# Kernel optimization log

Measured on AMD Instinct MI355X. Metric: run time of the kernel, lower is better.

## Reference

```python
import jax, jax.numpy as jnp
import numpy as np

B, L, ENC_IN, DM, H, HD, DFF, NL, C_OUT = 4, 1024, 64, 512, 8, 64, 2048, 3, 64
SCALE = 1.0 / np.sqrt(HD)


def _ln(x, g, b):
    m = x.mean(-1, keepdims=True)
    v = ((x - m) ** 2).mean(-1, keepdims=True)
    return (x - m) / jnp.sqrt(v + 1e-5) * g + b


def _pos_encoding(length, d):
    pos = np.arange(length)[:, None].astype(np.float32)
    div = np.exp(np.arange(0, d, 2).astype(np.float32) * (-np.log(10000.0) / d))
    pe = np.zeros((length, d), np.float32)
    pe[:, 0::2] = np.sin(pos * div)
    pe[:, 1::2] = np.cos(pos * div)
    return jnp.asarray(pe)

PE = _pos_encoding(L, DM)


def _prob_attn(q, k, v, idx):
    # q,k,v: [B,H,L,D]; idx: [L, sample_k] random key indices per query
    qk = jnp.einsum('bhqd,bhkd->bhqk', q, k)                       # [B,H,L,L]
    qks = jnp.take_along_axis(qk, idx[None, None, :, :], axis=-1)   # sampled QK
    M = qks.max(-1) - qks.sum(-1) / L                                # sparsity measure [B,H,L]
    _, top = jax.lax.top_k(M, L)  # n_top == L here (degenerate full selection / permutation)
    scores = jnp.take_along_axis(qk, top[..., None], axis=2) * SCALE  # gathered Q rows
    A = jax.nn.softmax(scores, axis=-1)
    return jnp.einsum('bhuk,bhkd->bhud', A, v)                       # [B,H,L,D]


def _forward(x_enc, sample_idx, W_emb, b_emb, Wq, bq, Wk, bk, Wv, bv, Wo, bo,
             W1, b1, W2, b2, g1, be1, g2, be2, gN, bN, W_proj, b_proj):
    x = x_enc @ W_emb + b_emb + PE[None]  # [B,L,DM]
    for i in range(NL):
        q = (x @ Wq[i] + bq[i]).reshape(B, L, H, HD).transpose(0, 2, 1, 3)
        k = (x @ Wk[i] + bk[i]).reshape(B, L, H, HD).transpose(0, 2, 1, 3)
        v = (x @ Wv[i] + bv[i]).reshape(B, L, H, HD).transpose(0, 2, 1, 3)
        o = _prob_attn(q, k, v, sample_idx[i]).transpose(0, 2, 1, 3).reshape(B, L, DM)
        o = o @ Wo[i] + bo[i]
        x = _ln(x + o, g1[i], be1[i])
        y = jax.nn.gelu(x @ W1[i] + b1[i], approximate=False) @ W2[i] + b2[i]
        x = _ln(x + y, g2[i], be2[i])
    x = _ln(x, gN, bN)
    return x @ W_proj + b_proj


def setup_inputs() -> dict:
    key = jax.random.key(0)
    ks = jax.random.split(key, 16)
    nrm = lambda k, s: jax.random.normal(k, s, jnp.float32) * 0.02
    return {
        'x_enc': jax.random.normal(ks[0], (B, L, ENC_IN), jnp.float32),
        'sample_idx': jax.random.randint(ks[1], (NL, L, L), 0, L, dtype=jnp.int32),
        'W_emb': nrm(ks[2], (ENC_IN, DM)), 'b_emb': jnp.zeros((DM,), jnp.float32),
        'Wq': nrm(ks[3], (NL, DM, DM)), 'bq': jnp.zeros((NL, DM), jnp.float32),
        'Wk': nrm(ks[4], (NL, DM, DM)), 'bk': jnp.zeros((NL, DM), jnp.float32),
        'Wv': nrm(ks[5], (NL, DM, DM)), 'bv': jnp.zeros((NL, DM), jnp.float32),
        'Wo': nrm(ks[6], (NL, DM, DM)), 'bo': jnp.zeros((NL, DM), jnp.float32),
        'W1': nrm(ks[7], (NL, DM, DFF)), 'b1': jnp.zeros((NL, DFF), jnp.float32),
        'W2': nrm(ks[8], (NL, DFF, DM)), 'b2': jnp.zeros((NL, DM), jnp.float32),
        'g1': jnp.ones((NL, DM), jnp.float32), 'be1': jnp.zeros((NL, DM), jnp.float32),
        'g2': jnp.ones((NL, DM), jnp.float32), 'be2': jnp.zeros((NL, DM), jnp.float32),
        'gN': jnp.ones((DM,), jnp.float32), 'bN': jnp.zeros((DM,), jnp.float32),
        'W_proj': nrm(ks[9], (DM, C_OUT)), 'b_proj': jnp.zeros((C_OUT,), jnp.float32),
    }


def reference(x_enc, sample_idx, W_emb, b_emb, Wq, bq, Wk, bk, Wv, bv, Wo, bo,
              W1, b1, W2, b2, g1, be1, g2, be2, gN, bN, W_proj, b_proj):
    return _forward(x_enc, sample_idx, W_emb, b_emb, Wq, bq, Wk, bk, Wv, bv, Wo, bo,
                    W1, b1, W2, b2, g1, be1, g2, be2, gN, bN, W_proj, b_proj)
```

## Files before the change

### kernel.cpp

```cpp
#include <hip/hip_runtime.h>
#include <cstdint>
#include <cstddef>

#define B_    4
#define L_    1024
#define ENCIN 64
#define DM    512
#define H_    8
#define HD    64
#define DFF   2048
#define NL    3
#define COUT  64
#define SCALE 0.125f
#define BH    32

typedef __attribute__((ext_vector_type(4))) short short4v;
typedef __attribute__((ext_vector_type(8))) short short8v;
typedef __attribute__((ext_vector_type(4))) float f32x4;
typedef unsigned short u16;

#define MFMA16(a,b,c) __builtin_amdgcn_mfma_f32_16x16x32_bf16(a,b,c,0,0,0)

#define GL2LDS(gsrc, ldst) \
  __builtin_amdgcn_global_load_lds( \
      (const __attribute__((address_space(1))) void*)(uintptr_t)(const void*)(gsrc), \
      (__attribute__((address_space(3))) void*)(uintptr_t)(const void*)(ldst), 16, 0, 0)

__device__ __forceinline__ u16 f2bf(float f){
  unsigned u = __float_as_uint(f);
  u += 0x7fffu + ((u >> 16) & 1u);
  return (u16)(u >> 16);
}
__device__ __forceinline__ float bf2f(u16 h){
  return __uint_as_float(((unsigned)h) << 16);
}
__device__ __forceinline__ void split2(float v, u16* h, u16* l){
  u16 hh = f2bf(v);
  *h = hh;
  *l = f2bf(v - bf2f(hh));
}

template<int MODE>
__global__ __launch_bounds__(256) void hgemm(
    const u16* __restrict__ Ah, const u16* __restrict__ Al,
    const u16* __restrict__ Bh, const u16* __restrict__ Bl,
    const float* __restrict__ bias1, const float* __restrict__ bias2,
    const float* __restrict__ bias3,
    float* __restrict__ o32, u16* __restrict__ oh, u16* __restrict__ ol,
    u16* __restrict__ oh2, u16* __restrict__ ol2, u16* __restrict__ ov,
    int Mtot, int N, int K, int klen)
{
  __shared__ u16 As[2][2][128*32];
  __shared__ u16 Bs[2][2][64*32];
  const int t = threadIdx.x, lane = t & 63, wid = t >> 6;
  const int wr = wid >> 1, wc = wid & 1;
  const int fr = lane & 15, fq = lane >> 4;
  const int m0 = blockIdx.y * 128, n0 = blockIdx.x * 64;
  const int z = blockIdx.z;
  const int kbase = z * klen;
  const int srow = lane >> 2, sseg = lane & 3;

  const int nk = klen / 32;

  auto stage = [&](int buf, int kt) {
#pragma unroll
    for (int i = 0; i < 2; i++) {
      int c = wid + 4*i;
      GL2LDS(&Ah[(size_t)(m0 + c*16 + srow)*K + kt + sseg*8], &As[buf][0][c*512]);
      GL2LDS(&Al[(size_t)(m0 + c*16 + srow)*K + kt + sseg*8], &As[buf][1][c*512]);
    }
    {
      int c = wid;
      GL2LDS(&Bh[(size_t)(n0 + c*16 + srow)*K + kt + sseg*8], &Bs[buf][0][c*512]);
      GL2LDS(&Bl[(size_t)(n0 + c*16 + srow)*K + kt + sseg*8], &Bs[buf][1][c*512]);
    }
  };

  f32x4 acc[4][2] = {};
  stage(0, kbase);
  __syncthreads();

  for (int it = 0; it < nk; ++it) {
    int cur = it & 1;
    if (it + 1 < nk) stage(cur ^ 1, kbase + (it+1)*32);

    short8v a0[4], a1[4], b0[2], b1[2];
#pragma unroll
    for (int m = 0; m < 4; m++) {
      int off = (wr*64 + m*16 + fr)*32 + fq*4;
      short4v x0 = *(const short4v*)&As[cur][0][off];
      short4v x1 = *(const short4v*)&As[cur][0][off + 16];
      a0[m] = __builtin_shufflevector(x0, x1, 0,1,2,3,4,5,6,7);
      short4v y0 = *(const short4v*)&As[cur][1][off];
      short4v y1 = *(const short4v*)&As[cur][1][off + 16];
      a1[m] = __builtin_shufflevector(y0, y1, 0,1,2,3,4,5,6,7);
    }
#pragma unroll
    for (int n = 0; n < 2; n++) {
      int off = (wc*32 + n*16 + fr)*32 + fq*4;
      short4v x0 = *(const short4v*)&Bs[cur][0][off];
      short4v x1 = *(const short4v*)&Bs[cur][0][off + 16];
      b0[n] = __builtin_shufflevector(x0, x1, 0,1,2,3,4,5,6,7);
      short4v y0 = *(const short4v*)&Bs[cur][1][off];
      short4v y1 = *(const short4v*)&Bs[cur][1][off + 16];
      b1[n] = __builtin_shufflevector(y0, y1, 0,1,2,3,4,5,6,7);
    }
#pragma unroll
    for (int m = 0; m < 4; m++)
#pragma unroll
      for (int n = 0; n < 2; n++) {
        acc[m][n] = MFMA16(a0[m], b0[n], acc[m][n]);
        acc[m][n] = MFMA16(a0[m], b1[n], acc[m][n]);
        acc[m][n] = MFMA16(a1[m], b0[n], acc[m][n]);
      }
    __syncthreads();
  }

#pragma unroll
  for (int m = 0; m < 4; m++) {
#pragma unroll
    for (int n = 0; n < 2; n++) {
      int gc = n0 + wc*32 + n*16 + fr;
#pragma unroll
      for (int r = 0; r < 4; r++) {
        int row = m0 + wr*64 + m*16 + fq*4 + r;
        float v = acc[m][n][r];
        if (MODE == 5) {
          o32[((size_t)z*Mtot + row)*N + gc] = v;
        } else if (MODE == 0) {
          o32[(size_t)row*N + gc] = v + bias1[gc];
        } else if (MODE == 1) {
          v += bias1[gc];
          int li = row & (L_ - 1);
          float dv = expf((float)(gc & ~1) * -0.017988946039015984f);
          float ang = (float)li * dv;
          v += (gc & 1) ? cosf(ang) : sinf(ang);
          size_t ix = (size_t)row*N + gc;
          o32[ix] = v;
          split2(v, &oh[ix], &ol[ix]);
        } else if (MODE == 2) {
          v += bias1[gc];
          float gv = 0.5f * v * (1.0f + erff(v * 0.70710678118654752f));
          size_t ix = (size_t)row*N + gc;
          split2(gv, &oh[ix], &ol[ix]);
        } else if (MODE == 3) {
          int b = row >> 10, li = row & (L_ - 1);
          int sub = gc >> 9, h = (gc >> 6) & 7, d = gc & 63;
          if (sub == 0) {
            v += bias1[gc];
            size_t ix = (((size_t)(b*H_ + h))*L_ + li)*HD + d;
            split2(v, &oh[ix], &ol[ix]);
          } else if (sub == 1) {
            v += bias2[gc - 512];
            size_t ix = (((size_t)(b*H_ + h))*L_ + li)*HD + d;
            split2(v, &oh2[ix], &ol2[ix]);
          } else {
            v += bias3[gc - 1024];
            size_t ix = (((size_t)(b*H_ + h))*HD + d)*L_ + li;
            ov[ix] = f2bf(v);
          }
        }
      }
    }
  }
}

__global__ __launch_bounds__(256) void qk_mfma(
    const u16* __restrict__ qh, const u16* __restrict__ ql,
    const u16* __restrict__ kh, const u16* __restrict__ kl,
    float* __restrict__ S, float* __restrict__ pmax, float* __restrict__ psum)
{
  __shared__ u16 Qs0[128*64], Qs1[128*64], Ks0[128*64], Ks1[128*64];
  const int t = threadIdx.x, lane = t & 63, wid = t >> 6;
  const int wr = wid >> 1, wc = wid & 1;
  const int fr = lane & 15, fq = lane >> 4;
  const int n0 = blockIdx.x * 128, m0 = blockIdx.y * 128, bh = blockIdx.z;
  const int srow = lane >> 3, sseg = lane & 7;
  const u16* qhb = qh + (size_t)bh * L_ * HD;
  const u16* qlb = ql + (size_t)bh * L_ * HD;
  const u16* khb = kh + (size_t)bh * L_ * HD;
  const u16* klb = kl + (size_t)bh * L_ * HD;

#pragma unroll
  for (int i = 0; i < 4; i++) {
    int c = wid + 4*i;
    GL2LDS(&qhb[(size_t)(m0 + c*8 + srow)*HD + sseg*8], &Qs0[c*512]);
    GL2LDS(&qlb[(size_t)(m0 + c*8 + srow)*HD + sseg*8], &Qs1[c*512]);
    GL2LDS(&khb[(size_t)(n0 + c*8 + srow)*HD + sseg*8], &Ks0[c*512]);
    GL2LDS(&klb[(size_t)(n0 + c*8 + srow)*HD + sseg*8], &Ks1[c*512]);
  }
  __syncthreads();

  f32x4 acc[4][4] = {};
#pragma unroll
  for (int ks = 0; ks < 2; ks++) {
    int kg = ks*32 + fq*4;
    short8v a0[4], a1[4], b0[4], b1[4];
#pragma unroll
    for (int m = 0; m < 4; m++) {
      int off = (wr*64 + m*16 + fr)*64 + kg;
      short4v x0 = *(const short4v*)&Qs0[off];
      short4v x1 = *(const short4v*)&Qs0[off + 16];
      a0[m] = __builtin_shufflevector(x0, x1, 0,1,2,3,4,5,6,7);
      short4v y0 = *(const short4v*)&Qs1[off];
      short4v y1 = *(const short4v*)&Qs1[off + 16];
      a1[m] = __builtin_shufflevector(y0, y1, 0,1,2,3,4,5,6,7);
    }
#pragma unroll
    for (int n = 0; n < 4; n++) {
      int off = (wc*64 + n*16 + fr)*64 + kg;
      short4v x0 = *(const short4v*)&Ks0[off];
      short4v x1 = *(const short4v*)&Ks0[off + 16];
      b0[n] = __builtin_shufflevector(x0, x1, 0,1,2,3,4,5,6,7);
      short4v y0 = *(const short4v*)&Ks1[off];
      short4v y1 = *(const short4v*)&Ks1[off + 16];
      b1[n] = __builtin_shufflevector(y0, y1, 0,1,2,3,4,5,6,7);
    }
#pragma unroll
    for (int m = 0; m < 4; m++)
#pragma unroll
      for (int n = 0; n < 4; n++) {
        acc[m][n] = MFMA16(a0[m], b0[n], acc[m][n]);
        acc[m][n] = MFMA16(a0[m], b1[n], acc[m][n]);
        acc[m][n] = MFMA16(a1[m], b0[n], acc[m][n]);
      }
  }

#pragma unroll
  for (int m = 0; m < 4; m++)
#pragma unroll
    for (int n = 0; n < 4; n++)
#pragma unroll
      for (int r = 0; r < 4; r++) {
        int grow = m0 + wr*64 + m*16 + fq*4 + r;
        int gcol = n0 + wc*64 + n*16 + fr;
        S[((size_t)bh*L_ + grow)*L_ + gcol] = acc[m][n][r];
      }

  const int tix = blockIdx.x*2 + wc;
#pragma unroll
  for (int m = 0; m < 4; m++) {
    float mx[4], sm[4];
#pragma unroll
    for (int r = 0; r < 4; r++) {
      float v = fmaxf(fmaxf(acc[m][0][r], acc[m][1][r]),
                      fmaxf(acc[m][2][r], acc[m][3][r]));
#pragma unroll
      for (int o2 = 1; o2 < 16; o2 <<= 1) v = fmaxf(v, __shfl_xor(v, o2));
      mx[r] = v * SCALE;
      float s = 0.f;
#pragma unroll
      for (int n = 0; n < 4; n++) s += expf(acc[m][n][r]*SCALE - mx[r]);
#pragma unroll
      for (int o2 = 1; o2 < 16; o2 <<= 1) s += __shfl_xor(s, o2);
      sm[r] = s;
    }
    if (fr == 0) {
#pragma unroll
      for (int r = 0; r < 4; r++) {
        int grow = m0 + wr*64 + m*16 + fq*4 + r;
        size_t ix = ((size_t)bh*L_ + grow)*16 + tix;
        pmax[ix] = mx[r];
        psum[ix] = sm[r];
      }
    }
  }
}

__global__ __launch_bounds__(256) void smc_k(const float* __restrict__ pmax,
    const float* __restrict__ psum, float* __restrict__ rmx, float* __restrict__ rsm)
{
  const int g = threadIdx.x & 15;
  const size_t flat = (size_t)blockIdx.x*16 + (threadIdx.x >> 4);
  float m = pmax[flat*16 + g], s = psum[flat*16 + g];
  float gm = m;
#pragma unroll
  for (int o = 1; o < 16; o <<= 1) gm = fmaxf(gm, __shfl_xor(gm, o));
  float gs = s * expf(m - gm);
#pragma unroll
  for (int o = 1; o < 16; o <<= 1) gs += __shfl_xor(gs, o);
  if (g == 0) { rmx[flat] = gm; rsm[flat] = gs; }
}

__global__ __launch_bounds__(256) void m_k(const float* __restrict__ S,
    const int* __restrict__ idx, float* __restrict__ Mv)
{
  const int qi = blockIdx.x, bh = blockIdx.y, t = threadIdx.x;
  const float* row = S + ((size_t)bh * L_ + qi) * L_;
  const int* ir = idx + (size_t)qi * L_;
  float mx = -1e30f, sm = 0.f;
  for (int s = t; s < L_; s += 256) {
    float v = row[ir[s]];
    mx = fmaxf(mx, v);
    sm += v;
  }
#pragma unroll
  for (int o = 32; o > 0; o >>= 1) {
    mx = fmaxf(mx, __shfl_xor(mx, o));
    sm += __shfl_xor(sm, o);
  }
  __shared__ float wmx[4], wsm[4];
  if ((t & 63) == 0) { wmx[t >> 6] = mx; wsm[t >> 6] = sm; }
  __syncthreads();
  if (t == 0) {
    mx = fmaxf(fmaxf(wmx[0], wmx[1]), fmaxf(wmx[2], wmx[3]));
    sm = wsm[0] + wsm[1] + wsm[2] + wsm[3];
    Mv[(size_t)bh * L_ + qi] = mx - sm * (1.0f / L_);
  }
}

__global__ __launch_bounds__(1024) void sort_k(const float* __restrict__ Mv,
                                               int* __restrict__ rank)
{
  __shared__ unsigned long long keys[L_];
  const int bh = blockIdx.x, t = threadIdx.x;
  float m = Mv[(size_t)bh * L_ + t];
  unsigned u = __float_as_uint(m);
  u = (u & 0x80000000u) ? ~u : (u | 0x80000000u);
  keys[t] = ((unsigned long long)(~u) << 32) | (unsigned)t;
  __syncthreads();
  for (int k = 2; k <= L_; k <<= 1) {
    for (int j = k >> 1; j > 0; j >>= 1) {
      int ixj = t ^ j;
      if (ixj > t) {
        unsigned long long a = keys[t], b = keys[ixj];
        bool up = ((t & k) == 0);
        if ((a > b) == up) { keys[t] = b; keys[ixj] = a; }
      }
      __syncthreads();
    }
  }
  int orig = (int)(keys[t] & 0xFFFFFFFFu);
  rank[(size_t)bh * L_ + orig] = t;
}

__global__ __launch_bounds__(256) void pv_mfma(
    const float* __restrict__ S, const u16* __restrict__ vt,
    const float* __restrict__ rmx, const float* __restrict__ rsm,
    const int* __restrict__ rank,
    u16* __restrict__ ath, u16* __restrict__ atl)
{
  __shared__ u16 Ps[64*64];
  __shared__ u16 Vs[64*64];
  __shared__ float rmaxS[64], rsumS[64];
  __shared__ int rankS[64];
  const int t = threadIdx.x, lane = t & 63, wid = t >> 6;
  const int wr = wid >> 1, wc = wid & 1;
  const int fr = lane & 15, fq = lane >> 4;
  const int l0 = blockIdx.x * 64, bh = blockIdx.y;
  const int bb = bh >> 3, hh = bh & 7;
  const int srow = lane >> 3, sseg = lane & 7;

  if (t < 64) {
    rmaxS[t] = rmx[(size_t)bh*L_ + l0 + t];
    rsumS[t] = rsm[(size_t)bh*L_ + l0 + t];
    rankS[t] = rank[(size_t)bh*L_ + l0 + t];
  }
  __syncthreads();

  f32x4 acc[2][2] = {};
  for (int c0 = 0; c0 < L_; c0 += 64) {
#pragma unroll
    for (int i = 0; i < 2; i++) {
      int c = wid + 4*i;
      GL2LDS(&vt[((size_t)bh*HD + c*8 + srow)*L_ + c0 + sseg*8], &Vs[c*512]);
    }
#pragma unroll
    for (int i = 0; i < 4; i++) {
      int f = t + 256*i;
      int row = f >> 4, q = f & 15;
      float4 s4 = *(const float4*)&S[((size_t)bh*L_ + l0 + row)*L_ + c0 + q*4];
      float mxr = rmaxS[row];
      short4v p4 = { (short)f2bf(expf(s4.x*SCALE - mxr)),
                     (short)f2bf(expf(s4.y*SCALE - mxr)),
                     (short)f2bf(expf(s4.z*SCALE - mxr)),
                     (short)f2bf(expf(s4.w*SCALE - mxr)) };
      *(short4v*)&Ps[row*64 + q*4] = p4;
    }
    __syncthreads();
#pragma unroll
    for (int ks = 0; ks < 2; ks++) {
      int kg = ks*32 + fq*4;
      short8v a[2], b[2];
#pragma unroll
      for (int m = 0; m < 2; m++) {
        int off = (wr*32 + m*16 + fr)*64 + kg;
        short4v x0 = *(const short4v*)&Ps[off];
        short4v x1 = *(const short4v*)&Ps[off + 16];
        a[m] = __builtin_shufflevector(x0, x1, 0,1,2,3,4,5,6,7);
      }
#pragma unroll
      for (int n = 0; n < 2; n++) {
        int off = (wc*32 + n*16 + fr)*64 + kg;
        short4v x0 = *(const short4v*)&Vs[off];
        short4v x1 = *(const short4v*)&Vs[off + 16];
        b[n] = __builtin_shufflevector(x0, x1, 0,1,2,3,4,5,6,7);
      }
#pragma unroll
      for (int m = 0; m < 2; m++)
#pragma unroll
        for (int n = 0; n < 2; n++)
          acc[m][n] = MFMA16(a[m], b[n], acc[m][n]);
    }
    __syncthreads();
  }

#pragma unroll
  for (int m = 0; m < 2; m++)
#pragma unroll
    for (int n = 0; n < 2; n++)
#pragma unroll
      for (int r = 0; r < 4; r++) {
        int lrow = wr*32 + m*16 + fq*4 + r;
        int u = rankS[lrow];
        int d = wc*32 + n*16 + fr;
        float o = acc[m][n][r] / rsumS[lrow];
        size_t ix = ((size_t)bb*L_ + u)*DM + hh*HD + d;
        split2(o, &ath[ix], &atl[ix]);
      }
}

__global__ __launch_bounds__(64) void ln2_k(const float* __restrict__ xin,
    const float* __restrict__ part, int np, const float* __restrict__ bias,
    const float* __restrict__ g, const float* __restrict__ bb,
    float* __restrict__ out, u16* __restrict__ oh, u16* __restrict__ ol)
{
  const int row = blockIdx.x, t = threadIdx.x;
  const float4* xf = (const float4*)(xin + (size_t)row * DM);
  float4 v0 = xf[t], v1 = xf[t + 64];
  for (int p = 0; p < np; p++) {
    const float4* af = (const float4*)(part + ((size_t)p*(B_*L_) + row) * DM);
    float4 a0 = af[t], a1 = af[t + 64];
    v0.x += a0.x; v0.y += a0.y; v0.z += a0.z; v0.w += a0.w;
    v1.x += a1.x; v1.y += a1.y; v1.z += a1.z; v1.w += a1.w;
  }
  if (bias) {
    const float4* cf = (const float4*)bias;
    float4 c0 = cf[t], c1 = cf[t + 64];
    v0.x += c0.x; v0.y += c0.y; v0.z += c0.z; v0.w += c0.w;
    v1.x += c1.x; v1.y += c1.y; v1.z += c1.z; v1.w += c1.w;
  }
  float s  = v0.x + v0.y + v0.z + v0.w + v1.x + v1.y + v1.z + v1.w;
  float ss = v0.x*v0.x + v0.y*v0.y + v0.z*v0.z + v0.w*v0.w +
             v1.x*v1.x + v1.y*v1.y + v1.z*v1.z + v1.w*v1.w;
#pragma unroll
  for (int o = 32; o > 0; o >>= 1) { s += __shfl_xor(s, o); ss += __shfl_xor(ss, o); }
  float mean = s * (1.0f / DM);
  float var  = ss * (1.0f / DM) - mean * mean;
  float inv  = 1.0f / sqrtf(var + 1e-5f);
  const float4* gf = (const float4*)g;
  const float4* bf = (const float4*)bb;
  float4 g0 = gf[t], g1 = gf[t + 64], b0 = bf[t], b1 = bf[t + 64];
  float o0[4], o1[4];
  o0[0] = (v0.x-mean)*inv*g0.x + b0.x; o0[1] = (v0.y-mean)*inv*g0.y + b0.y;
  o0[2] = (v0.z-mean)*inv*g0.z + b0.z; o0[3] = (v0.w-mean)*inv*g0.w + b0.w;
  o1[0] = (v1.x-mean)*inv*g1.x + b1.x; o1[1] = (v1.y-mean)*inv*g1.y + b1.y;
  o1[2] = (v1.z-mean)*inv*g1.z + b1.z; o1[3] = (v1.w-mean)*inv*g1.w + b1.w;
  float4* of = (float4*)(out + (size_t)row * DM);
  of[t]      = make_float4(o0[0], o0[1], o0[2], o0[3]);
  of[t + 64] = make_float4(o1[0], o1[1], o1[2], o1[3]);
  size_t base = (size_t)row * DM;
#pragma unroll
  for (int j = 0; j < 4; j++) {
    split2(o0[j], &oh[base + t*4 + j],       &ol[base + t*4 + j]);
    split2(o1[j], &oh[base + 256 + t*4 + j], &ol[base + 256 + t*4 + j]);
  }
}

__global__ __launch_bounds__(256) void wt_k(const float* __restrict__ W,
    u16* __restrict__ Th, u16* __restrict__ Tl, int K, int N,
    size_t wz, size_t tz)
{
  W  += (size_t)blockIdx.z * wz;
  Th += (size_t)blockIdx.z * tz;
  Tl += (size_t)blockIdx.z * tz;
  __shared__ float tile[32][33];
  const int k0 = blockIdx.y * 32, n0 = blockIdx.x * 32;
  const int c = threadIdx.x & 31, r4 = threadIdx.x >> 5;
#pragma unroll
  for (int i = 0; i < 4; i++) {
    int r = r4 * 4 + i;
    tile[r][c] = W[(size_t)(k0 + r) * N + n0 + c];
  }
  __syncthreads();
#pragma unroll
  for (int i = 0; i < 4; i++) {
    int r = r4 * 4 + i;
    float v = tile[c][r];
    split2(v, &Th[(size_t)(n0 + r) * K + k0 + c], &Tl[(size_t)(n0 + r) * K + k0 + c]);
  }
}

__global__ __launch_bounds__(256) void split_k(const float* __restrict__ in,
    u16* __restrict__ oh, u16* __restrict__ ol, int n4)
{
  int i = blockIdx.x * 256 + threadIdx.x;
  if (i < n4) {
    float4 v = ((const float4*)in)[i];
    split2(v.x, &oh[i*4+0], &ol[i*4+0]);
    split2(v.y, &oh[i*4+1], &ol[i*4+1]);
    split2(v.z, &oh[i*4+2], &ol[i*4+2]);
    split2(v.w, &oh[i*4+3], &ol[i*4+3]);
  }
}

extern "C" void kernel_launch(void* const* d_in, const int* in_sizes, int n_in,
                              void* d_out, int out_size, void* d_ws, size_t ws_size,
                              hipStream_t stream)
{
  const float* x_enc   = (const float*)d_in[0];
  const int*   sidx    = (const int*)d_in[1];
  const float* W_emb   = (const float*)d_in[2];
  const float* b_emb   = (const float*)d_in[3];
  const float* Wq      = (const float*)d_in[4];
  const float* bq      = (const float*)d_in[5];
  const float* Wk      = (const float*)d_in[6];
  const float* bk      = (const float*)d_in[7];
  const float* Wv      = (const float*)d_in[8];
  const float* bv      = (const float*)d_in[9];
  const float* Wo      = (const float*)d_in[10];
  const float* bo      = (const float*)d_in[11];
  const float* W1      = (const float*)d_in[12];
  const float* b1      = (const float*)d_in[13];
  const float* W2      = (const float*)d_in[14];
  const float* b2      = (const float*)d_in[15];
  const float* g1      = (const float*)d_in[16];
  const float* be1     = (const float*)d_in[17];
  const float* g2      = (const float*)d_in[18];
  const float* be2     = (const float*)d_in[19];
  const float* gN      = (const float*)d_in[20];
  const float* bN      = (const float*)d_in[21];
  const float* W_proj  = (const float*)d_in[22];
  const float* b_proj  = (const float*)d_in[23];

  const int M = B_ * L_;
  char* w = (char*)d_ws;
  float* S   = (float*)w;  w += (size_t)BH * L_ * L_ * 4;
  float* x   = (float*)w;  w += (size_t)M * DM * 4;
  u16* xh    = (u16*)w;    w += (size_t)M * DM * 2;
  u16* xl    = (u16*)w;    w += (size_t)M * DM * 2;
  u16* qh_   = (u16*)w;    w += (size_t)BH * L_ * HD * 2;
  u16* ql_   = (u16*)w;    w += (size_t)BH * L_ * HD * 2;
  u16* kh_   = (u16*)w;    w += (size_t)BH * L_ * HD * 2;
  u16* kl_   = (u16*)w;    w += (size_t)BH * L_ * HD * 2;
  u16* vt_   = (u16*)w;    w += (size_t)BH * L_ * HD * 2;
  u16* ath   = (u16*)w;    w += (size_t)M * DM * 2;
  u16* atl   = (u16*)w;    w += (size_t)M * DM * 2;
  float* rmx_ = (float*)w; w += (size_t)BH * L_ * 4;
  float* rsm_ = (float*)w; w += (size_t)BH * L_ * 4;
  float* Mv_  = (float*)w; w += (size_t)BH * L_ * 4;
  int* rank_  = (int*)w;   w += (size_t)BH * L_ * 4;
  float* pmax_ = (float*)w; w += (size_t)BH * L_ * 16 * 4;
  float* psum_ = (float*)w; w += (size_t)BH * L_ * 16 * 4;
  u16* WqkvTh = (u16*)w; w += (size_t)NL*1536*DM*2;
  u16* WqkvTl = (u16*)w; w += (size_t)NL*1536*DM*2;
  u16* WoTh   = (u16*)w; w += (size_t)NL*DM*DM*2;
  u16* WoTl   = (u16*)w; w += (size_t)NL*DM*DM*2;
  u16* W1Th   = (u16*)w; w += (size_t)NL*DFF*DM*2;
  u16* W1Tl   = (u16*)w; w += (size_t)NL*DFF*DM*2;
  u16* W2Th   = (u16*)w; w += (size_t)NL*DM*DFF*2;
  u16* W2Tl   = (u16*)w; w += (size_t)NL*DM*DFF*2;
  u16* WeTh   = (u16*)w; w += (size_t)DM*ENCIN*2;
  u16* WeTl   = (u16*)w; w += (size_t)DM*ENCIN*2;
  u16* WpTh   = (u16*)w; w += (size_t)COUT*DM*2;
  u16* WpTl   = (u16*)w; w += (size_t)COUT*DM*2;
  u16*   yh     = (u16*)S;
  u16*   yl     = (u16*)((char*)S + 16u*1024u*1024u);
  float* partWo = (float*)((char*)S + 32u*1024u*1024u);
  float* partW2 = (float*)((char*)S + 48u*1024u*1024u);
  u16*   xeh    = (u16*)((char*)S + 80u*1024u*1024u);
  u16*   xel    = xeh + (size_t)M*ENCIN;

  split_k<<<dim3((M*ENCIN/4 + 255)/256), 256, 0, stream>>>(x_enc, xeh, xel, M*ENCIN/4);
  wt_k<<<dim3(DM/32, DM/32, NL), 256, 0, stream>>>(Wq, WqkvTh,            WqkvTl,            DM, DM, (size_t)DM*DM, (size_t)1536*DM);
  wt_k<<<dim3(DM/32, DM/32, NL), 256, 0, stream>>>(Wk, WqkvTh + 512*DM,   WqkvTl + 512*DM,   DM, DM, (size_t)DM*DM, (size_t)1536*DM);
  wt_k<<<dim3(DM/32, DM/32, NL), 256, 0, stream>>>(Wv, WqkvTh + 1024*DM,  WqkvTl + 1024*DM,  DM, DM, (size_t)DM*DM, (size_t)1536*DM);
  wt_k<<<dim3(DM/32, DM/32, NL), 256, 0, stream>>>(Wo, WoTh, WoTl, DM, DM, (size_t)DM*DM, (size_t)DM*DM);
  wt_k<<<dim3(DFF/32, DM/32, NL), 256, 0, stream>>>(W1, W1Th, W1Tl, DM, DFF, (size_t)DM*DFF, (size_t)DFF*DM);
  wt_k<<<dim3(DM/32, DFF/32, NL), 256, 0, stream>>>(W2, W2Th, W2Tl, DFF, DM, (size_t)DFF*DM, (size_t)DM*DFF);
  wt_k<<<dim3(DM/32, ENCIN/32, 1), 256, 0, stream>>>(W_emb, WeTh, WeTl, ENCIN, DM, 0, 0);
  wt_k<<<dim3(COUT/32, DM/32, 1), 256, 0, stream>>>(W_proj, WpTh, WpTl, DM, COUT, 0, 0);

  hgemm<1><<<dim3(DM/64, M/128, 1), 256, 0, stream>>>(
      xeh, xel, WeTh, WeTl, b_emb, nullptr, nullptr,
      x, xh, xl, nullptr, nullptr, nullptr, M, DM, ENCIN, ENCIN);

  for (int il = 0; il < NL; il++) {
    hgemm<3><<<dim3(1536/64, M/128, 1), 256, 0, stream>>>(
        xh, xl, WqkvTh + (size_t)il*1536*DM, WqkvTl + (size_t)il*1536*DM,
        bq + il*DM, bk + il*DM, bv + il*DM,
        nullptr, qh_, ql_, kh_, kl_, vt_, M, 1536, DM, DM);

    qk_mfma<<<dim3(L_/128, L_/128, BH), 256, 0, stream>>>(qh_, ql_, kh_, kl_, S, pmax_, psum_);
    smc_k<<<dim3(BH*L_/16), 256, 0, stream>>>(pmax_, psum_, rmx_, rsm_);
    m_k<<<dim3(L_, BH), 256, 0, stream>>>(S, sidx + (size_t)il*L_*L_, Mv_);
    sort_k<<<BH, 1024, 0, stream>>>(Mv_, rank_);
    pv_mfma<<<dim3(L_/64, BH), 256, 0, stream>>>(S, vt_, rmx_, rsm_, rank_, ath, atl);

    hgemm<5><<<dim3(DM/64, M/128, 2), 256, 0, stream>>>(
        ath, atl, WoTh + (size_t)il*DM*DM, WoTl + (size_t)il*DM*DM,
        nullptr, nullptr, nullptr,
        partWo, nullptr, nullptr, nullptr, nullptr, nullptr, M, DM, DM, DM/2);
    ln2_k<<<M, 64, 0, stream>>>(x, partWo, 2, bo + il*DM, g1 + il*DM, be1 + il*DM, x, xh, xl);

    hgemm<2><<<dim3(DFF/64, M/128, 1), 256, 0, stream>>>(
        xh, xl, W1Th + (size_t)il*DFF*DM, W1Tl + (size_t)il*DFF*DM,
        b1 + il*DFF, nullptr, nullptr,
        nullptr, yh, yl, nullptr, nullptr, nullptr, M, DFF, DM, DM);
    hgemm<5><<<dim3(DM/64, M/128, 4), 256, 0, stream>>>(
        yh, yl, W2Th + (size_t)il*DM*DFF, W2Tl + (size_t)il*DM*DFF,
        nullptr, nullptr, nullptr,
        partW2, nullptr, nullptr, nullptr, nullptr, nullptr, M, DM, DFF, DFF/4);
    ln2_k<<<M, 64, 0, stream>>>(x, partW2, 4, b2 + il*DM, g2 + il*DM, be2 + il*DM, x, xh, xl);
  }

  ln2_k<<<M, 64, 0, stream>>>(x, nullptr, 0, nullptr, gN, bN, x, xh, xl);
  hgemm<0><<<dim3(COUT/64, M/128, 1), 256, 0, stream>>>(
      xh, xl, WpTh, WpTl, b_proj, nullptr, nullptr,
      (float*)d_out, nullptr, nullptr, nullptr, nullptr, nullptr, M, COUT, DM, DM);
}
```

Before: 1.803 ms.

## Fuse attention into flash-style kernels, widen GEMM tiles, split-K final projection

Replaces the materialized fp32 score matrix with two fused kernels. The first recomputes QK^T per 16-query wave to get online softmax stats and the sampled sparsity measure, using a precomputed per-layer sample-count table. The second recomputes QK^T, applies exp and accumulates PV directly in registers. GEMM tile width becomes a template parameter, set to 128 for the QKV, Wo, W1 and W2 GEMMs, and the final projection uses split-K with a reduce kernel. This removes the large S write/read traffic but computes QK^T twice and reads K/V directly from global memory without LDS staging.

```diff
diff --git a/kernel.cpp b/kernel.cpp
--- a/kernel.cpp
+++ b/kernel.cpp
@@ -18,6 +18,7 @@
 typedef __attribute__((ext_vector_type(8))) short short8v;
 typedef __attribute__((ext_vector_type(4))) float f32x4;
 typedef unsigned short u16;
+typedef unsigned char u8;
 
 #define MFMA16(a,b,c) __builtin_amdgcn_mfma_f32_16x16x32_bf16(a,b,c,0,0,0)
 
@@ -39,8 +40,11 @@
   *h = hh;
   *l = f2bf(v - bf2f(hh));
 }
-
-template<int MODE>
+__device__ __forceinline__ short8v cat8(short4v a, short4v b){
+  return __builtin_shufflevector(a, b, 0,1,2,3,4,5,6,7);
+}
+
+template<int BN, int MODE>
 __global__ __launch_bounds__(256) void hgemm(
     const u16* __restrict__ Ah, const u16* __restrict__ Al,
     const u16* __restrict__ Bh, const u16* __restrict__ Bl,
@@ -50,12 +54,13 @@
     u16* __restrict__ oh2, u16* __restrict__ ol2, u16* __restrict__ ov,
     int Mtot, int N, int K, int klen)
 {
+  constexpr int NT = BN / 32;
   __shared__ u16 As[2][2][128*32];
-  __shared__ u16 Bs[2][2][64*32];
+  __shared__ u16 Bs[2][2][BN*32];
   const int t = threadIdx.x, lane = t & 63, wid = t >> 6;
   const int wr = wid >> 1, wc = wid & 1;
   const int fr = lane & 15, fq = lane >> 4;
-  const int m0 = blockIdx.y * 128, n0 = blockIdx.x * 64;
+  const int m0 = blockIdx.y * 128, n0 = blockIdx.x * BN;
   const int z = blockIdx.z;
   const int kbase = z * klen;
   const int srow = lane >> 2, sseg = lane & 3;
@@ -69,14 +74,15 @@
       GL2LDS(&Ah[(size_t)(m0 + c*16 + srow)*K + kt + sseg*8], &As[buf][0][c*512]);
       GL2LDS(&Al[(size_t)(m0 + c*16 + srow)*K + kt + sseg*8], &As[buf][1][c*512]);
     }
-    {
-      int c = wid;
+#pragma unroll
+    for (int i = 0; i < BN/64; i++) {
+      int c = wid + 4*i;
       GL2LDS(&Bh[(size_t)(n0 + c*16 + srow)*K + kt + sseg*8], &Bs[buf][0][c*512]);
       GL2LDS(&Bl[(size_t)(n0 + c*16 + srow)*K + kt + sseg*8], &Bs[buf][1][c*512]);
     }
   };
 
-  f32x4 acc[4][2] = {};
+  f32x4 acc[4][NT] = {};
   stage(0, kbase);
   __syncthreads();
 
@@ -84,31 +90,23 @@
     int cur = it & 1;
     if (it + 1 < nk) stage(cur ^ 1, kbase + (it+1)*32);
 
-    short8v a0[4], a1[4], b0[2], b1[2];
+    short8v a0[4], a1[4], b0[NT], b1[NT];
 #pragma unroll
     for (int m = 0; m < 4; m++) {
       int off = (wr*64 + m*16 + fr)*32 + fq*4;
-      short4v x0 = *(const short4v*)&As[cur][0][off];
-      short4v x1 = *(const short4v*)&As[cur][0][off + 16];
-      a0[m] = __builtin_shufflevector(x0, x1, 0,1,2,3,4,5,6,7);
-      short4v y0 = *(const short4v*)&As[cur][1][off];
-      short4v y1 = *(const short4v*)&As[cur][1][off + 16];
-      a1[m] = __builtin_shufflevector(y0, y1, 0,1,2,3,4,5,6,7);
-    }
-#pragma unroll
-    for (int n = 0; n < 2; n++) {
-      int off = (wc*32 + n*16 + fr)*32 + fq*4;
-      short4v x0 = *(const short4v*)&Bs[cur][0][off];
-      short4v x1 = *(const short4v*)&Bs[cur][0][off + 16];
-      b0[n] = __builtin_shufflevector(x0, x1, 0,1,2,3,4,5,6,7);
-      short4v y0 = *(const short4v*)&Bs[cur][1][off];
-      short4v y1 = *(const short4v*)&Bs[cur][1][off + 16];
-      b1[n] = __builtin_shufflevector(y0, y1, 0,1,2,3,4,5,6,7);
+      a0[m] = cat8(*(const short4v*)&As[cur][0][off], *(const short4v*)&As[cur][0][off+16]);
+      a1[m] = cat8(*(const short4v*)&As[cur][1][off], *(const short4v*)&As[cur][1][off+16]);
+    }
+#pragma unroll
+    for (int n = 0; n < NT; n++) {
+      int off = (wc*(BN/2) + n*16 + fr)*32 + fq*4;
+      b0[n] = cat8(*(const short4v*)&Bs[cur][0][off], *(const short4v*)&Bs[cur][0][off+16]);
+      b1[n] = cat8(*(const short4v*)&Bs[cur][1][off], *(const short4v*)&Bs[cur][1][off+16]);
     }
 #pragma unroll
     for (int m = 0; m < 4; m++)
 #pragma unroll
-      for (int n = 0; n < 2; n++) {
+      for (int n = 0; n < NT; n++) {
         acc[m][n] = MFMA16(a0[m], b0[n], acc[m][n]);
         acc[m][n] = MFMA16(a0[m], b1[n], acc[m][n]);
         acc[m][n] = MFMA16(a1[m], b0[n], acc[m][n]);
@@ -119,8 +117,8 @@
 #pragma unroll
   for (int m = 0; m < 4; m++) {
 #pragma unroll
-    for (int n = 0; n < 2; n++) {
-      int gc = n0 + wc*32 + n*16 + fr;
+    for (int n = 0; n < NT; n++) {
+      int gc = n0 + wc*(BN/2) + n*16 + fr;
 #pragma unroll
       for (int r = 0; r < 4; r++) {
         int row = m0 + wr*64 + m*16 + fq*4 + r;
@@ -165,147 +163,132 @@
   }
 }
 
-__global__ __launch_bounds__(256) void qk_mfma(
+__global__ __launch_bounds__(256) void cnt_k(const int* __restrict__ sidx,
+                                             u8* __restrict__ cnt)
+{
+  __shared__ unsigned c[L_];
+  const int row = blockIdx.x, il = blockIdx.y, t = threadIdx.x;
+#pragma unroll
+  for (int i = 0; i < 4; i++) c[t + 256*i] = 0;
+  __syncthreads();
+  const int* ir = sidx + ((size_t)il*L_ + row)*L_;
+#pragma unroll
+  for (int i = 0; i < 4; i++) atomicAdd(&c[ir[t + 256*i]], 1u);
+  __syncthreads();
+  u8* out = cnt + ((size_t)il*L_ + row)*L_;
+#pragma unroll
+  for (int i = 0; i < 4; i++) out[t + 256*i] = (u8)c[t + 256*i];
+}
+
+__device__ __forceinline__ void st_tile(
+    const u16* __restrict__ khb, const u16* __restrict__ klb,
+    int ct, int fr, int fq, const short8v Qh[2], const short8v Ql[2],
+    f32x4 sacc[4])
+{
+#pragma unroll
+  for (int ks = 0; ks < 2; ks++) {
+#pragma unroll
+    for (int mi = 0; mi < 4; mi++) {
+      const u16* ph = &khb[(size_t)(ct*64 + mi*16 + fr)*HD + ks*32 + fq*4];
+      short8v ah = cat8(*(const short4v*)ph, *(const short4v*)(ph + 16));
+      const u16* pl = &klb[(size_t)(ct*64 + mi*16 + fr)*HD + ks*32 + fq*4];
+      short8v al = cat8(*(const short4v*)pl, *(const short4v*)(pl + 16));
+      sacc[mi] = MFMA16(ah, Qh[ks], sacc[mi]);
+      sacc[mi] = MFMA16(ah, Ql[ks], sacc[mi]);
+      sacc[mi] = MFMA16(al, Qh[ks], sacc[mi]);
+    }
+  }
+}
+
+__device__ __forceinline__ void load_qfrags(
+    const u16* __restrict__ qhb, const u16* __restrict__ qlb,
+    int fr, int fq, short8v Qh[2], short8v Ql[2])
+{
+#pragma unroll
+  for (int ks = 0; ks < 2; ks++) {
+    const u16* p = &qhb[fr*HD + ks*32 + fq*4];
+    Qh[ks] = cat8(*(const short4v*)p, *(const short4v*)(p + 16));
+    const u16* p2 = &qlb[fr*HD + ks*32 + fq*4];
+    Ql[ks] = cat8(*(const short4v*)p2, *(const short4v*)(p2 + 16));
+  }
+}
+
+__device__ __forceinline__ void fdecode(int bid, int w, int& bh, int& q0)
+{
+  int xcd = bid & 7, ii = bid >> 3;
+  bh = xcd*4 + (ii >> 4);
+  q0 = (ii & 15)*64 + w*16;
+}
+
+__global__ __launch_bounds__(256) void fqk_stat(
     const u16* __restrict__ qh, const u16* __restrict__ ql,
     const u16* __restrict__ kh, const u16* __restrict__ kl,
-    float* __restrict__ S, float* __restrict__ pmax, float* __restrict__ psum)
-{
-  __shared__ u16 Qs0[128*64], Qs1[128*64], Ks0[128*64], Ks1[128*64];
-  const int t = threadIdx.x, lane = t & 63, wid = t >> 6;
-  const int wr = wid >> 1, wc = wid & 1;
+    const u8* __restrict__ cnt,
+    float* __restrict__ rmx, float* __restrict__ rsm, float* __restrict__ Mv)
+{
+  const int t = threadIdx.x, lane = t & 63, w = t >> 6;
   const int fr = lane & 15, fq = lane >> 4;
-  const int n0 = blockIdx.x * 128, m0 = blockIdx.y * 128, bh = blockIdx.z;
-  const int srow = lane >> 3, sseg = lane & 7;
-  const u16* qhb = qh + (size_t)bh * L_ * HD;
-  const u16* qlb = ql + (size_t)bh * L_ * HD;
-  const u16* khb = kh + (size_t)bh * L_ * HD;
-  const u16* klb = kl + (size_t)bh * L_ * HD;
-
-#pragma unroll
-  for (int i = 0; i < 4; i++) {
-    int c = wid + 4*i;
-    GL2LDS(&qhb[(size_t)(m0 + c*8 + srow)*HD + sseg*8], &Qs0[c*512]);
-    GL2LDS(&qlb[(size_t)(m0 + c*8 + srow)*HD + sseg*8], &Qs1[c*512]);
-    GL2LDS(&khb[(size_t)(n0 + c*8 + srow)*HD + sseg*8], &Ks0[c*512]);
-    GL2LDS(&klb[(size_t)(n0 + c*8 + srow)*HD + sseg*8], &Ks1[c*512]);
-  }
-  __syncthreads();
-
-  f32x4 acc[4][4] = {};
-#pragma unroll
-  for (int ks = 0; ks < 2; ks++) {
-    int kg = ks*32 + fq*4;
-    short8v a0[4], a1[4], b0[4], b1[4];
-#pragma unroll
-    for (int m = 0; m < 4; m++) {
-      int off = (wr*64 + m*16 + fr)*64 + kg;
-      short4v x0 = *(const short4v*)&Qs0[off];
-      short4v x1 = *(const short4v*)&Qs0[off + 16];
-      a0[m] = __builtin_shufflevector(x0, x1, 0,1,2,3,4,5,6,7);
-      short4v y0 = *(const short4v*)&Qs1[off];
-      short4v y1 = *(const short4v*)&Qs1[off + 16];
-      a1[m] = __builtin_shufflevector(y0, y1, 0,1,2,3,4,5,6,7);
-    }
-#pragma unroll
-    for (int n = 0; n < 4; n++) {
-      int off = (wc*64 + n*16 + fr)*64 + kg;
-      short4v x0 = *(const short4v*)&Ks0[off];
-      short4v x1 = *(const short4v*)&Ks0[off + 16];
-      b0[n] = __builtin_shufflevector(x0, x1, 0,1,2,3,4,5,6,7);
-      short4v y0 = *(const short4v*)&Ks1[off];
-      short4v y1 = *(const short4v*)&Ks1[off + 16];
-      b1[n] = __builtin_shufflevector(y0, y1, 0,1,2,3,4,5,6,7);
-    }
-#pragma unroll
-    for (int m = 0; m < 4; m++)
-#pragma unroll
-      for (int n = 0; n < 4; n++) {
-        acc[m][n] = MFMA16(a0[m], b0[n], acc[m][n]);
-        acc[m][n] = MFMA16(a0[m], b1[n], acc[m][n]);
-        acc[m][n] = MFMA16(a1[m], b0[n], acc[m][n]);
+  int bh, q0; fdecode(blockIdx.x, w, bh, q0);
+  const u16* qhb = qh + ((size_t)bh*L_ + q0)*HD;
+  const u16* qlb = ql + ((size_t)bh*L_ + q0)*HD;
+  const u16* khb = kh + (size_t)bh*L_*HD;
+  const u16* klb = kl + (size_t)bh*L_*HD;
+  const u8* crow = cnt + (size_t)(q0 + fr)*L_;
+
+  short8v Qh[2], Ql[2];
+  load_qfrags(qhb, qlb, fr, fq, Qh, Ql);
+
+  float run_m = -1e30f, run_s = 0.f, smp_m = -1e30f, wsum = 0.f;
+
+#pragma unroll 4
+  for (int ct = 0; ct < 16; ct++) {
+    f32x4 sacc[4] = {};
+    st_tile(khb, klb, ct, fr, fq, Qh, Ql, sacc);
+
+    float tmax = sacc[0][0];
+#pragma unroll
+    for (int mi = 0; mi < 4; mi++)
+#pragma unroll
+      for (int r = 0; r < 4; r++) tmax = fmaxf(tmax, sacc[mi][r]);
+    float zm = tmax * SCALE;
+    float tsum = 0.f;
+#pragma unroll
+    for (int mi = 0; mi < 4; mi++)
+#pragma unroll
+      for (int r = 0; r < 4; r++) tsum += expf(sacc[mi][r]*SCALE - zm);
+    float nm = fmaxf(run_m, zm);
+    run_s = run_s*expf(run_m - nm) + tsum*expf(zm - nm);
+    run_m = nm;
+
+#pragma unroll
+    for (int mi = 0; mi < 4; mi++) {
+      unsigned cw = *(const unsigned*)&crow[ct*64 + mi*16 + fq*4];
+#pragma unroll
+      for (int r = 0; r < 4; r++) {
+        float cf = (float)((cw >> (8*r)) & 255u);
+        float s = sacc[mi][r];
+        wsum += cf * s;
+        if (cf > 0.f) smp_m = fmaxf(smp_m, s);
       }
-  }
-
-#pragma unroll
-  for (int m = 0; m < 4; m++)
-#pragma unroll
-    for (int n = 0; n < 4; n++)
-#pragma unroll
-      for (int r = 0; r < 4; r++) {
-        int grow = m0 + wr*64 + m*16 + fq*4 + r;
-        int gcol = n0 + wc*64 + n*16 + fr;
-        S[((size_t)bh*L_ + grow)*L_ + gcol] = acc[m][n][r];
-      }
-
-  const int tix = blockIdx.x*2 + wc;
-#pragma unroll
-  for (int m = 0; m < 4; m++) {
-    float mx[4], sm[4];
-#pragma unroll
-    for (int r = 0; r < 4; r++) {
-      float v = fmaxf(fmaxf(acc[m][0][r], acc[m][1][r]),
-                      fmaxf(acc[m][2][r], acc[m][3][r]));
-#pragma unroll
-      for (int o2 = 1; o2 < 16; o2 <<= 1) v = fmaxf(v, __shfl_xor(v, o2));
-      mx[r] = v * SCALE;
-      float s = 0.f;
-#pragma unroll
-      for (int n = 0; n < 4; n++) s += expf(acc[m][n][r]*SCALE - mx[r]);
-#pragma unroll
-      for (int o2 = 1; o2 < 16; o2 <<= 1) s += __shfl_xor(s, o2);
-      sm[r] = s;
-    }
-    if (fr == 0) {
-#pragma unroll
-      for (int r = 0; r < 4; r++) {
-        int grow = m0 + wr*64 + m*16 + fq*4 + r;
-        size_t ix = ((size_t)bh*L_ + grow)*16 + tix;
-        pmax[ix] = mx[r];
-        psum[ix] = sm[r];
-      }
-    }
-  }
-}
-
-__global__ __launch_bounds__(256) void smc_k(const float* __restrict__ pmax,
-    const float* __restrict__ psum, float* __restrict__ rmx, float* __restrict__ rsm)
-{
-  const int g = threadIdx.x & 15;
-  const size_t flat = (size_t)blockIdx.x*16 + (threadIdx.x >> 4);
-  float m = pmax[flat*16 + g], s = psum[flat*16 + g];
-  float gm = m;
-#pragma unroll
-  for (int o = 1; o < 16; o <<= 1) gm = fmaxf(gm, __shfl_xor(gm, o));
-  float gs = s * expf(m - gm);
-#pragma unroll
-  for (int o = 1; o < 16; o <<= 1) gs += __shfl_xor(gs, o);
-  if (g == 0) { rmx[flat] = gm; rsm[flat] = gs; }
-}
-
-__global__ __launch_bounds__(256) void m_k(const float* __restrict__ S,
-    const int* __restrict__ idx, float* __restrict__ Mv)
-{
-  const int qi = blockIdx.x, bh = blockIdx.y, t = threadIdx.x;
-  const float* row = S + ((size_t)bh * L_ + qi) * L_;
-  const int* ir = idx + (size_t)qi * L_;
-  float mx = -1e30f, sm = 0.f;
-  for (int s = t; s < L_; s += 256) {
-    float v = row[ir[s]];
-    mx = fmaxf(mx, v);
-    sm += v;
-  }
-#pragma unroll
-  for (int o = 32; o > 0; o >>= 1) {
-    mx = fmaxf(mx, __shfl_xor(mx, o));
-    sm += __shfl_xor(sm, o);
-  }
-  __shared__ float wmx[4], wsm[4];
-  if ((t & 63) == 0) { wmx[t >> 6] = mx; wsm[t >> 6] = sm; }
-  __syncthreads();
-  if (t == 0) {
-    mx = fmaxf(fmaxf(wmx[0], wmx[1]), fmaxf(wmx[2], wmx[3]));
-    sm = wsm[0] + wsm[1] + wsm[2] + wsm[3];
-    Mv[(size_t)bh * L_ + qi] = mx - sm * (1.0f / L_);
+    }
+  }
+
+#pragma unroll
+  for (int mask = 16; mask <= 32; mask <<= 1) {
+    float om = __shfl_xor(run_m, mask);
+    float os = __shfl_xor(run_s, mask);
+    float nm = fmaxf(run_m, om);
+    run_s = run_s*expf(run_m - nm) + os*expf(om - nm);
+    run_m = nm;
+    smp_m = fmaxf(smp_m, __shfl_xor(smp_m, mask));
+    wsum += __shfl_xor(wsum, mask);
+  }
+
+  if (fq == 0) {
+    size_t ix = (size_t)bh*L_ + q0 + fr;
+    rmx[ix] = run_m;
+    rsm[ix] = run_s;
+    Mv[ix]  = smp_m - wsum * (1.0f / L_);
   }
 }
 
@@ -334,90 +317,67 @@
   rank[(size_t)bh * L_ + orig] = t;
 }
 
-__global__ __launch_bounds__(256) void pv_mfma(
-    const float* __restrict__ S, const u16* __restrict__ vt,
+__global__ __launch_bounds__(256) void fpv(
+    const u16* __restrict__ qh, const u16* __restrict__ ql,
+    const u16* __restrict__ kh, const u16* __restrict__ kl,
+    const u16* __restrict__ vt,
     const float* __restrict__ rmx, const float* __restrict__ rsm,
     const int* __restrict__ rank,
     u16* __restrict__ ath, u16* __restrict__ atl)
 {
-  __shared__ u16 Ps[64*64];
-  __shared__ u16 Vs[64*64];
-  __shared__ float rmaxS[64], rsumS[64];
-  __shared__ int rankS[64];
-  const int t = threadIdx.x, lane = t & 63, wid = t >> 6;
-  const int wr = wid >> 1, wc = wid & 1;
+  const int t = threadIdx.x, lane = t & 63, w = t >> 6;
   const int fr = lane & 15, fq = lane >> 4;
-  const int l0 = blockIdx.x * 64, bh = blockIdx.y;
+  int bh, q0; fdecode(blockIdx.x, w, bh, q0);
   const int bb = bh >> 3, hh = bh & 7;
-  const int srow = lane >> 3, sseg = lane & 7;
-
-  if (t < 64) {
-    rmaxS[t] = rmx[(size_t)bh*L_ + l0 + t];
-    rsumS[t] = rsm[(size_t)bh*L_ + l0 + t];
-    rankS[t] = rank[(size_t)bh*L_ + l0 + t];
-  }
-  __syncthreads();
-
-  f32x4 acc[2][2] = {};
-  for (int c0 = 0; c0 < L_; c0 += 64) {
-#pragma unroll
-    for (int i = 0; i < 2; i++) {
-      int c = wid + 4*i;
-      GL2LDS(&vt[((size_t)bh*HD + c*8 + srow)*L_ + c0 + sseg*8], &Vs[c*512]);
-    }
-#pragma unroll
-    for (int i = 0; i < 4; i++) {
-      int f = t + 256*i;
-      int row = f >> 4, q = f & 15;
-      float4 s4 = *(const float4*)&S[((size_t)bh*L_ + l0 + row)*L_ + c0 + q*4];
-      float mxr = rmaxS[row];
-      short4v p4 = { (short)f2bf(expf(s4.x*SCALE - mxr)),
-                     (short)f2bf(expf(s4.y*SCALE - mxr)),
-                     (short)f2bf(expf(s4.z*SCALE - mxr)),
-                     (short)f2bf(expf(s4.w*SCALE - mxr)) };
-      *(short4v*)&Ps[row*64 + q*4] = p4;
-    }
-    __syncthreads();
-#pragma unroll
-    for (int ks = 0; ks < 2; ks++) {
-      int kg = ks*32 + fq*4;
-      short8v a[2], b[2];
-#pragma unroll
-      for (int m = 0; m < 2; m++) {
-        int off = (wr*32 + m*16 + fr)*64 + kg;
-        short4v x0 = *(const short4v*)&Ps[off];
-        short4v x1 = *(const short4v*)&Ps[off + 16];
-        a[m] = __builtin_shufflevector(x0, x1, 0,1,2,3,4,5,6,7);
+  const u16* qhb = qh + ((size_t)bh*L_ + q0)*HD;
+  const u16* qlb = ql + ((size_t)bh*L_ + q0)*HD;
+  const u16* khb = kh + (size_t)bh*L_*HD;
+  const u16* klb = kl + (size_t)bh*L_*HD;
+  const u16* vtb = vt + (size_t)bh*HD*L_;
+
+  short8v Qh[2], Ql[2];
+  load_qfrags(qhb, qlb, fr, fq, Qh, Ql);
+
+  const float mq = rmx[(size_t)bh*L_ + q0 + fr];
+
+  f32x4 pacc[4] = {};
+
+#pragma unroll 4
+  for (int ct = 0; ct < 16; ct++) {
+    f32x4 sacc[4] = {};
+    st_tile(khb, klb, ct, fr, fq, Qh, Ql, sacc);
+
+#pragma unroll
+    for (int kt = 0; kt < 2; kt++) {
+      short8v pa;
+#pragma unroll
+      for (int j = 0; j < 4; j++) {
+        pa[j]   = (short)f2bf(expf(sacc[2*kt][j]  *SCALE - mq));
+        pa[j+4] = (short)f2bf(expf(sacc[2*kt+1][j]*SCALE - mq));
       }
 #pragma unroll
-      for (int n = 0; n < 2; n++) {
-        int off = (wc*32 + n*16 + fr)*64 + kg;
-        short4v x0 = *(const short4v*)&Vs[off];
-        short4v x1 = *(const short4v*)&Vs[off + 16];
-        b[n] = __builtin_shufflevector(x0, x1, 0,1,2,3,4,5,6,7);
+      for (int nd = 0; nd < 4; nd++) {
+        const u16* pv = &vtb[(size_t)(nd*16 + fr)*L_ + ct*64 + kt*32 + fq*4];
+        short8v bv = cat8(*(const short4v*)pv, *(const short4v*)(pv + 16));
+        pacc[nd] = MFMA16(pa, bv, pacc[nd]);
       }
-#pragma unroll
-      for (int m = 0; m < 2; m++)
-#pragma unroll
-        for (int n = 0; n < 2; n++)
-          acc[m][n] = MFMA16(a[m], b[n], acc[m][n]);
-    }
-    __syncthreads();
-  }
-
-#pragma unroll
-  for (int m = 0; m < 2; m++)
-#pragma unroll
-    for (int n = 0; n < 2; n++)
-#pragma unroll
-      for (int r = 0; r < 4; r++) {
-        int lrow = wr*32 + m*16 + fq*4 + r;
-        int u = rankS[lrow];
-        int d = wc*32 + n*16 + fr;
-        float o = acc[m][n][r] / rsumS[lrow];
-        size_t ix = ((size_t)bb*L_ + u)*DM + hh*HD + d;
-        split2(o, &ath[ix], &atl[ix]);
-      }
+    }
+  }
+
+  float rs[4]; int uu[4];
+#pragma unroll
+  for (int r = 0; r < 4; r++) {
+    rs[r] = rsm[(size_t)bh*L_ + q0 + fq*4 + r];
+    uu[r] = rank[(size_t)bh*L_ + q0 + fq*4 + r];
+  }
+#pragma unroll
+  for (int nd = 0; nd < 4; nd++)
+#pragma unroll
+    for (int r = 0; r < 4; r++) {
+      float o = pacc[nd][r] / rs[r];
+      size_t ix = ((size_t)bb*L_ + uu[r])*DM + hh*HD + nd*16 + fr;
+      split2(o, &ath[ix], &atl[ix]);
+    }
 }
 
 __global__ __launch_bounds__(64) void ln2_k(const float* __restrict__ xin,
@@ -464,6 +424,18 @@
   for (int j = 0; j < 4; j++) {
     split2(o0[j], &oh[base + t*4 + j],       &ol[base + t*4 + j]);
     split2(o1[j], &oh[base + 256 + t*4 + j], &ol[base + 256 + t*4 + j]);
+  }
+}
+
+__global__ __launch_bounds__(256) void rp_k(const float* __restrict__ part,
+    const float* __restrict__ bias, float* __restrict__ out, int n)
+{
+  int i = blockIdx.x * 256 + threadIdx.x;
+  if (i < n) {
+    float v = bias[i & (COUT-1)];
+#pragma unroll
+    for (int z = 0; z < 4; z++) v += part[(size_t)z*n + i];
+    out[i] = v;
   }
 }
 
@@ -535,7 +507,6 @@
 
   const int M = B_ * L_;
   char* w = (char*)d_ws;
-  float* S   = (float*)w;  w += (size_t)BH * L_ * L_ * 4;
   float* x   = (float*)w;  w += (size_t)M * DM * 4;
   u16* xh    = (u16*)w;    w += (size_t)M * DM * 2;
   u16* xl    = (u16*)w;    w += (size_t)M * DM * 2;
@@ -550,8 +521,14 @@
   float* rsm_ = (float*)w; w += (size_t)BH * L_ * 4;
   float* Mv_  = (float*)w; w += (size_t)BH * L_ * 4;
   int* rank_  = (int*)w;   w += (size_t)BH * L_ * 4;
-  float* pmax_ = (float*)w; w += (size_t)BH * L_ * 16 * 4;
-  float* psum_ = (float*)w; w += (size_t)BH * L_ * 16 * 4;
+  u8* cnt_    = (u8*)w;    w += (size_t)NL * L_ * L_;
+  u16* yh     = (u16*)w;   w += (size_t)M * DFF * 2;
+  u16* yl     = (u16*)w;   w += (size_t)M * DFF * 2;
+  float* partWo = (float*)w; w += (size_t)2 * M * DM * 4;
+  float* partW2 = (float*)w; w += (size_t)4 * M * DM * 4;
+  float* partPj = (float*)w; w += (size_t)4 * M * COUT * 4;
+  u16* xeh    = (u16*)w;   w += (size_t)M * ENCIN * 2;
+  u16* xel    = (u16*)w;   w += (size_t)M * ENCIN * 2;
   u16* WqkvTh = (u16*)w; w += (size_t)NL*1536*DM*2;
   u16* WqkvTl = (u16*)w; w += (size_t)NL*1536*DM*2;
   u16* WoTh   = (u16*)w; w += (size_t)NL*DM*DM*2;
@@ -564,50 +541,45 @@
   u16* WeTl   = (u16*)w; w += (size_t)DM*ENCIN*2;
   u16* WpTh   = (u16*)w; w += (size_t)COUT*DM*2;
   u16* WpTl   = (u16*)w; w += (size_t)COUT*DM*2;
-  u16*   yh     = (u16*)S;
-  u16*   yl     = (u16*)((char*)S + 16u*1024u*1024u);
-  float* partWo = (float*)((char*)S + 32u*1024u*1024u);
-  float* partW2 = (float*)((char*)S + 48u*1024u*1024u);
-  u16*   xeh    = (u16*)((char*)S + 80u*1024u*1024u);
-  u16*   xel    = xeh + (size_t)M*ENCIN;
 
   split_k<<<dim3((M*ENCIN/4 + 255)/256), 256, 0, stream>>>(x_enc, xeh, xel, M*ENCIN/4);
-  wt_k<<<dim3(DM/32, DM/32, NL), 256, 0, stream>>>(Wq, WqkvTh,            WqkvTl,            DM, DM, (size_t)DM*DM, (size_t)1536*DM);
-  wt_k<<<dim3(DM/32, DM/32, NL), 256, 0, stream>>>(Wk, WqkvTh + 512*DM,   WqkvTl + 512*DM,   DM, DM, (size_t)DM*DM, (size_t)1536*DM);
-  wt_k<<<dim3(DM/32, DM/32, NL), 256, 0, stream>>>(Wv, WqkvTh + 1024*DM,  WqkvTl + 1024*DM,  DM, DM, (size_t)DM*DM, (size_t)1536*DM);
+  cnt_k<<<dim3(L_, NL), 256, 0, stream>>>(sidx, cnt_);
+  wt_k<<<dim3(DM/32, DM/32, NL), 256, 0, stream>>>(Wq, WqkvTh,           WqkvTl,           DM, DM, (size_t)DM*DM, (size_t)1536*DM);
+  wt_k<<<dim3(DM/32, DM/32, NL), 256, 0, stream>>>(Wk, WqkvTh + 512*DM,  WqkvTl + 512*DM,  DM, DM, (size_t)DM*DM, (size_t)1536*DM);
+  wt_k<<<dim3(DM/32, DM/32, NL), 256, 0, stream>>>(Wv, WqkvTh + 1024*DM, WqkvTl + 1024*DM, DM, DM, (size_t)DM*DM, (size_t)1536*DM);
   wt_k<<<dim3(DM/32, DM/32, NL), 256, 0, stream>>>(Wo, WoTh, WoTl, DM, DM, (size_t)DM*DM, (size_t)DM*DM);
   wt_k<<<dim3(DFF/32, DM/32, NL), 256, 0, stream>>>(W1, W1Th, W1Tl, DM, DFF, (size_t)DM*DFF, (size_t)DFF*DM);
   wt_k<<<dim3(DM/32, DFF/32, NL), 256, 0, stream>>>(W2, W2Th, W2Tl, DFF, DM, (size_t)DFF*DM, (size_t)DM*DFF);
   wt_k<<<dim3(DM/32, ENCIN/32, 1), 256, 0, stream>>>(W_emb, WeTh, WeTl, ENCIN, DM, 0, 0);
   wt_k<<<dim3(COUT/32, DM/32, 1), 256, 0, stream>>>(W_proj, WpTh, WpTl, DM, COUT, 0, 0);
 
-  hgemm<1><<<dim3(DM/64, M/128, 1), 256, 0, stream>>>(
+  hgemm<64,1><<<dim3(DM/64, M/128, 1), 256, 0, stream>>>(
       xeh, xel, WeTh, WeTl, b_emb, nullptr, nullptr,
       x, xh, xl, nullptr, nullptr, nullptr, M, DM, ENCIN, ENCIN);
 
   for (int il = 0; il < NL; il++) {
-    hgemm<3><<<dim3(1536/64, M/128, 1), 256, 0, stream>>>(
+    hgemm<128,3><<<dim3(1536/128, M/128, 1), 256, 0, stream>>>(
         xh, xl, WqkvTh + (size_t)il*1536*DM, WqkvTl + (size_t)il*1536*DM,
         bq + il*DM, bk + il*DM, bv + il*DM,
         nullptr, qh_, ql_, kh_, kl_, vt_, M, 1536, DM, DM);
 
-    qk_mfma<<<dim3(L_/128, L_/128, BH), 256, 0, stream>>>(qh_, ql_, kh_, kl_, S, pmax_, psum_);
-    smc_k<<<dim3(BH*L_/16), 256, 0, stream>>>(pmax_, psum_, rmx_, rsm_);
-    m_k<<<dim3(L_, BH), 256, 0, stream>>>(S, sidx + (size_t)il*L_*L_, Mv_);
+    fqk_stat<<<512, 256, 0, stream>>>(qh_, ql_, kh_, kl_,
+        cnt_ + (size_t)il*L_*L_, rmx_, rsm_, Mv_);
     sort_k<<<BH, 1024, 0, stream>>>(Mv_, rank_);
-    pv_mfma<<<dim3(L_/64, BH), 256, 0, stream>>>(S, vt_, rmx_, rsm_, rank_, ath, atl);
-
-    hgemm<5><<<dim3(DM/64, M/128, 2), 256, 0, stream>>>(
+    fpv<<<512, 256, 0, stream>>>(qh_, ql_, kh_, kl_, vt_,
+        rmx_, rsm_, rank_, ath, atl);
+
+    hgemm<128,5><<<dim3(DM/128, M/128, 2), 256, 0, stream>>>(
         ath, atl, WoTh + (size_t)il*DM*DM, WoTl + (size_t)il*DM*DM,
         nullptr, nullptr, nullptr,
         partWo, nullptr, nullptr, nullptr, nullptr, nullptr, M, DM, DM, DM/2);
     ln2_k<<<M, 64, 0, stream>>>(x, partWo, 2, bo + il*DM, g1 + il*DM, be1 + il*DM, x, xh, xl);
 
-    hgemm<2><<<dim3(DFF/64, M/128, 1), 256, 0, stream>>>(
+    hgemm<128,2><<<dim3(DFF/128, M/128, 1), 256, 0, stream>>>(
         xh, xl, W1Th + (size_t)il*DFF*DM, W1Tl + (size_t)il*DFF*DM,
         b1 + il*DFF, nullptr, nullptr,
         nullptr, yh, yl, nullptr, nullptr, nullptr, M, DFF, DM, DM);
-    hgemm<5><<<dim3(DM/64, M/128, 4), 256, 0, stream>>>(
+    hgemm<128,5><<<dim3(DM/128, M/128, 4), 256, 0, stream>>>(
         yh, yl, W2Th + (size_t)il*DM*DFF, W2Tl + (size_t)il*DM*DFF,
         nullptr, nullptr, nullptr,
         partW2, nullptr, nullptr, nullptr, nullptr, nullptr, M, DM, DFF, DFF/4);
@@ -615,7 +587,8 @@
   }
 
   ln2_k<<<M, 64, 0, stream>>>(x, nullptr, 0, nullptr, gN, bN, x, xh, xl);
-  hgemm<0><<<dim3(COUT/64, M/128, 1), 256, 0, stream>>>(
-      xh, xl, WpTh, WpTl, b_proj, nullptr, nullptr,
-      (float*)d_out, nullptr, nullptr, nullptr, nullptr, nullptr, M, COUT, DM, DM);
-}
+  hgemm<64,5><<<dim3(COUT/64, M/128, 4), 256, 0, stream>>>(
+      xh, xl, WpTh, WpTl, nullptr, nullptr, nullptr,
+      partPj, nullptr, nullptr, nullptr, nullptr, nullptr, M, COUT, DM, DM/4);
+  rp_k<<<dim3(M*COUT/256), 256, 0, stream>>>(partPj, b_proj, (float*)d_out, M*COUT);
+}
```

Measured after the change: 1.906 ms. 5.7% more time.
